# Optimization experiments

Measured on AMD Instinct MI355X. Metric: run time of the kernel, lower is better.

## Reference

```python
import jax, jax.numpy as jnp
import numpy as np

L1 = 512
LX = 32
COUNT = 8


def setup_inputs() -> dict:
    key = jax.random.key(0)
    ks = jax.random.split(key, 9)
    B = 65536
    x = jax.random.uniform(ks[0], (B, 2 * L1), dtype=jnp.float32)  # NNUE accumulator is in [0,1]
    ls_indices = jax.random.randint(ks[1], (B,), 0, COUNT, dtype=jnp.int64)
    # params (scaled ~1/sqrt(fan_in))
    w_fact = jax.random.normal(ks[2], (LX, 2 * L1), dtype=jnp.float32) * (1.0 / np.sqrt(2 * L1))
    w0 = jax.random.normal(ks[3], (LX * COUNT, 2 * L1), dtype=jnp.float32) * (1.0 / np.sqrt(2 * L1))
    b0 = jax.random.normal(ks[4], (LX * COUNT,), dtype=jnp.float32) * 0.05
    w1 = jax.random.normal(ks[5], (LX * COUNT, LX), dtype=jnp.float32) * (1.0 / np.sqrt(LX))
    b1 = jax.random.normal(ks[6], (LX * COUNT,), dtype=jnp.float32) * 0.05
    w2 = jax.random.normal(ks[7], (1 * COUNT, LX), dtype=jnp.float32) * (1.0 / np.sqrt(LX))
    b2 = jax.random.normal(ks[8], (1 * COUNT,), dtype=jnp.float32) * 0.05
    return {"x": x, "ls_indices": ls_indices, "w_fact": w_fact,
            "w0": w0, "b0": b0, "w1": w1, "b1": b1, "w2": w2, "b2": b2}


def _stack_linear_gather(h, w, b, idx, out_dim):
    # dense Linear for all COUNT buckets, then gather the selected bucket per row
    y = (h @ w.T + b).reshape(-1, COUNT, out_dim)          # [B, COUNT, out_dim]
    return y.reshape(-1, out_dim)[idx]                      # [B, out_dim]


def reference(x, ls_indices, w_fact, w0, b0, w1, b1, w2, b2):
    B = x.shape[0]
    idx = ls_indices.astype(jnp.int32) + jnp.arange(B, dtype=jnp.int32) * COUNT
    l1f = x @ w_fact.T                                      # [B, LX]
    h = _stack_linear_gather(x, w0, b0, idx, LX) + l1f      # layer 0 + factorized term
    h = jnp.clip(h, 0.0, 1.0)
    h = _stack_linear_gather(h, w1, b1, idx, LX)            # hidden layer 1
    h = jnp.clip(h, 0.0, 1.0)
    out = _stack_linear_gather(h, w2, b2, idx, 1)           # output layer (no clamp)
    return out
```

## Files before the change

### kernel.cpp

```cpp
#include <hip/hip_runtime.h>


#define B_ROWS 65536
#define LK     1024
#define TILE   32
#define MAIN_BLOCKS (B_ROWS / TILE + 8)
#define SROW   2056

#define SORTED_OFF 1024
#define WB_OFF     (1024 + 131072)

typedef short  short8  __attribute__((ext_vector_type(8)));
typedef float  f32x16  __attribute__((ext_vector_type(16)));

__device__ __forceinline__ unsigned pkbf(float a, float b) {
    unsigned ua = __float_as_uint(a), ub = __float_as_uint(b);
    ua = (ua + 0x7FFFu + ((ua >> 16) & 1u)) >> 16;
    ub = (ub + 0x7FFFu + ((ub >> 16) & 1u)) >> 16;
    return (ua & 0xFFFFu) | (ub << 16);
}

__device__ __forceinline__ bool detect_i64(const int* p) {
    int acc = 0;
#pragma unroll
    for (int i = 0; i < 64; ++i) acc |= p[2 * i + 1];
    return acc == 0;
}

__device__ __forceinline__ int load_bucket(const int* p, int r, bool i64) {
    return (i64 ? p[2 * r] : p[r]) & 7;
}

__global__ __launch_bounds__(1024) void k_prep(
    const int* __restrict__ idx, const float* __restrict__ w0,
    const float* __restrict__ wf, uint4* __restrict__ wB,
    unsigned short* __restrict__ sorted, int* __restrict__ hdr)
{
    int t = threadIdx.x;

    if (blockIdx.x > 0) {
        int f = (blockIdx.x - 1) * 1024 + t;
        int b   = f >> 12;
        int i12 = f & 4095;
        int kc  = i12 >> 8;
        int i8  = i12 & 255;
        int n   = i8 & 31;
        int khi = i8 >> 5;
        int k = kc * 64 + khi * 8;
        const float* p0 = w0 + (size_t)(b * 32 + n) * LK + k;
        const float* pf = wf + (size_t)n * LK + k;
        float v[8];
#pragma unroll
        for (int j = 0; j < 8; ++j) v[j] = p0[j] + pf[j];
        uint4 o;
        o.x = pkbf(v[0], v[1]); o.y = pkbf(v[2], v[3]);
        o.z = pkbf(v[4], v[5]); o.w = pkbf(v[6], v[7]);
        wB[f] = o;
        return;
    }

    __shared__ int wcnt[16][8];
    __shared__ int wbase[16][8];
    __shared__ int segb[8];

    bool i64 = detect_i64(idx);
    int wv = t >> 6, lane = t & 63;
    int rowbase = wv * 4096;

    unsigned nib[8] = {0, 0, 0, 0, 0, 0, 0, 0};
    int c[8] = {0, 0, 0, 0, 0, 0, 0, 0};
#pragma unroll 8
    for (int i = 0; i < 64; ++i) {
        int r = rowbase + i * 64 + lane;
        int b = load_bucket(idx, r, i64);
        nib[i >> 3] |= (unsigned)b << (4 * (i & 7));
#pragma unroll
        for (int bb = 0; bb < 8; ++bb) c[bb] += (b == bb) ? 1 : 0;
    }
#pragma unroll
    for (int bb = 0; bb < 8; ++bb) {
        int v = c[bb];
#pragma unroll
        for (int s = 1; s < 64; s <<= 1) v += __shfl_xor(v, s);
        if (lane == 0) wcnt[wv][bb] = v;
    }
    __syncthreads();

    if (t == 0) {
        int base = 0, tt = 0;
        for (int b = 0; b < 8; ++b) {
            int tot = 0;
            for (int w = 0; w < 16; ++w) tot += wcnt[w][b];
            hdr[b] = tot; hdr[16 + b] = base; hdr[24 + b] = tt;
            segb[b] = base;
            base += tot;
            tt += (tot + TILE - 1) / TILE;
        }
        hdr[24 + 8] = tt;
    }
    __syncthreads();

    if (t < 128) {
        int w2 = t >> 3, b = t & 7;
        int base = segb[b];
        for (int w = 0; w < w2; ++w) base += wcnt[w][b];
        wbase[w2][b] = base;
    }
    __syncthreads();

    int mycur = (lane < 8) ? wbase[wv][lane] : 0;
#pragma unroll
    for (int i = 0; i < 64; ++i) {
        int b = (nib[i >> 3] >> (4 * (i & 7))) & 7;
        unsigned long long mown = 0;
        int addc = 0;
#pragma unroll
        for (int bb = 0; bb < 8; ++bb) {
            unsigned long long m = __ballot(b == bb);
            if (b == bb) mown = m;
            if (lane == bb) addc = __popcll(m);
        }
        int base = __shfl(mycur, b);
        int rank = __popcll(mown & ((1ull << lane) - 1ull));
        sorted[base + rank] = (unsigned short)(rowbase + i * 64 + lane);
        mycur += addc;
    }
}

__global__ __launch_bounds__(256, 2) void k_main(
    const float* __restrict__ x, const unsigned short* __restrict__ sorted,
    const int* __restrict__ hdr, const uint4* __restrict__ wB,
    const float* __restrict__ b0, const float* __restrict__ w1,
    const float* __restrict__ b1, const float* __restrict__ w2,
    const float* __restrict__ b2, float* __restrict__ out)
{
    __shared__ __align__(16) unsigned char smem[TILE * SROW];
    float* rbuf = (float*)smem;
    float* hb   = (float*)(smem + 16384);

    int total = hdr[24 + 8];
    int g = blockIdx.x;
    if (g >= total) return;

    int bkt = 0;
    while (bkt < 7 && hdr[24 + bkt + 1] <= g) bkt++;
    int tile  = g - hdr[24 + bkt];
    int cnt   = hdr[bkt];
    int seg   = hdr[16 + bkt];
    int p0    = seg + tile * TILE;
    int nrows = min(TILE, cnt - tile * TILE);

    int t    = threadIdx.x;
    int lane = t & 63;
    int wv   = t >> 6;

#pragma unroll
    for (int j0 = 0; j0 < 32; j0 += 8) {
        float4 v[8];
#pragma unroll
        for (int jj = 0; jj < 8; ++jj) {
            int j = j0 + jj;
            int gr = (int)sorted[p0 + min(j, nrows - 1)];
            v[jj] = ((const float4*)(x + (size_t)gr * LK))[t];
        }
#pragma unroll
        for (int jj = 0; jj < 8; ++jj) {
            int j = j0 + jj;
            uint2 o;
            o.x = pkbf(v[jj].x, v[jj].y);
            o.y = pkbf(v[jj].z, v[jj].w);
            *(uint2*)(smem + j * SROW + t * 8) = o;
        }
    }
    __syncthreads();

    const uint4* wBg = wB + (size_t)bkt * 4096;
    const unsigned char* Abase = smem + (size_t)(lane & 31) * SROW + 16 * (lane >> 5);

    f32x16 acc;
#pragma unroll
    for (int i = 0; i < 16; ++i) acc[i] = 0.0f;

    union UA { uint2 h[2]; short8 s; };
    union UB { uint4 u;    short8 s; };
#pragma unroll
    for (int cc = 0; cc < 16; ++cc) {
        int c = wv * 16 + cc;
        UA ua;
        ua.h[0] = *(const uint2*)(Abase + 32 * c);
        ua.h[1] = *(const uint2*)(Abase + 32 * c + 8);
        UB ub;
        ub.u = wBg[c * 64 + lane];
        acc = __builtin_amdgcn_mfma_f32_32x32x16_bf16(ua.s, ub.s, acc, 0, 0, 0);
    }

    __syncthreads();
#pragma unroll
    for (int r = 0; r < 16; ++r)
        rbuf[wv * 1024 + r * 64 + lane] = acc[r];
    __syncthreads();

#pragma unroll
    for (int q = 0; q < 4; ++q) {
        int e = t + 256 * q;
        float s = rbuf[e] + rbuf[1024 + e] + rbuf[2048 + e] + rbuf[3072 + e];
        int rr = e >> 6, ll = e & 63;
        int m = (rr & 3) + 8 * (rr >> 2) + 4 * (ll >> 5);
        int n = ll & 31;
        float h = s + b0[bkt * 32 + n];
        h = fminf(fmaxf(h, 0.0f), 1.0f);
        hb[m * 36 + n] = h;
    }
    __syncthreads();

    if (t < 64) {
        int r = t >> 1, half = t & 1;
        const float4* hr = (const float4*)(hb + r * 36);
        float4 ha[8];
#pragma unroll
        for (int q = 0; q < 8; ++q) ha[q] = hr[q];
        const float* w1b = w1 + (size_t)bkt * 1024;
        const float* b1b = b1 + bkt * 32;
        const float* w2b = w2 + bkt * 32;
        float partial = 0.0f;
#pragma unroll
        for (int jj = 0; jj < 16; ++jj) {
            int j2 = half * 16 + jj;
            const float4* wr = (const float4*)&w1b[j2 * 32];
            float s = b1b[j2];
#pragma unroll
            for (int q = 0; q < 8; ++q) {
                float4 w4 = wr[q];
                s += ha[q].x * w4.x + ha[q].y * w4.y + ha[q].z * w4.z + ha[q].w * w4.w;
            }
            s = fminf(fmaxf(s, 0.0f), 1.0f);
            partial += s * w2b[j2];
        }
        partial += __shfl_xor(partial, 1);
        if (half == 0 && r < nrows) {
            int gr = (int)sorted[p0 + r];
            out[gr] = partial + b2[bkt];
        }
    }
}

extern "C" void kernel_launch(void* const* d_in, const int* in_sizes, int n_in,
                              void* d_out, int out_size, void* d_ws, size_t ws_size,
                              hipStream_t stream) {
    const float* x   = (const float*)d_in[0];
    const int*   lsi = (const int*)  d_in[1];
    const float* wf  = (const float*)d_in[2];
    const float* w0  = (const float*)d_in[3];
    const float* b0  = (const float*)d_in[4];
    const float* w1  = (const float*)d_in[5];
    const float* b1  = (const float*)d_in[6];
    const float* w2  = (const float*)d_in[7];
    const float* b2  = (const float*)d_in[8];
    float* out = (float*)d_out;

    char* ws = (char*)d_ws;
    int* hdr = (int*)ws;
    unsigned short* sorted = (unsigned short*)(ws + SORTED_OFF);
    uint4* wB = (uint4*)(ws + WB_OFF);

    k_prep<<<33, 1024, 0, stream>>>(lsi, w0, wf, wB, sorted, hdr);
    k_main<<<MAIN_BLOCKS, 256, 0, stream>>>(x, sorted, hdr, wB,
                                            b0, w1, b1, w2, b2, out);
}
```

Before: 439.1 us.

## Compute all buckets per tile in natural row order, dropping bucket sort

Removes the per-call bucket counting and sort of rows in the prep kernel. Each main-kernel block now processes 32 consecutive rows: every wave computes two buckets' layer-0 outputs over the full K, and each row keeps only its own bucket's result. This trades 8x more MFMA work and a full-K loop per wave for contiguous x loads, no gather, and no single-block sort step on the critical path. It also removes the cross-wave LDS reduction.

```diff
diff --git a/kernel.cpp b/kernel.cpp
--- a/kernel.cpp
+++ b/kernel.cpp
@@ -4,11 +4,9 @@
 #define B_ROWS 65536
 #define LK     1024
 #define TILE   32
-#define MAIN_BLOCKS (B_ROWS / TILE + 8)
+#define NBLK   (B_ROWS / TILE)
 #define SROW   2056
 
-#define SORTED_OFF 1024
-#define WB_OFF     (1024 + 131072)
 
 typedef short  short8  __attribute__((ext_vector_type(8)));
 typedef float  f32x16  __attribute__((ext_vector_type(16)));
@@ -32,189 +30,104 @@
 }
 
 __global__ __launch_bounds__(1024) void k_prep(
-    const int* __restrict__ idx, const float* __restrict__ w0,
-    const float* __restrict__ wf, uint4* __restrict__ wB,
-    unsigned short* __restrict__ sorted, int* __restrict__ hdr)
+    const float* __restrict__ w0, const float* __restrict__ wf,
+    uint4* __restrict__ wB)
 {
-    int t = threadIdx.x;
-
-    if (blockIdx.x > 0) {
-        int f = (blockIdx.x - 1) * 1024 + t;
-        int b   = f >> 12;
-        int i12 = f & 4095;
-        int kc  = i12 >> 8;
-        int i8  = i12 & 255;
-        int n   = i8 & 31;
-        int khi = i8 >> 5;
-        int k = kc * 64 + khi * 8;
-        const float* p0 = w0 + (size_t)(b * 32 + n) * LK + k;
-        const float* pf = wf + (size_t)n * LK + k;
-        float v[8];
+    int f = blockIdx.x * 1024 + threadIdx.x;
+    int b   = f >> 12;
+    int i12 = f & 4095;
+    int kc  = i12 >> 8;
+    int i8  = i12 & 255;
+    int n   = i8 & 31;
+    int khi = i8 >> 5;
+    int k = kc * 64 + khi * 8;
+    const float* p0 = w0 + (size_t)(b * 32 + n) * LK + k;
+    const float* pf = wf + (size_t)n * LK + k;
+    float v[8];
 #pragma unroll
-        for (int j = 0; j < 8; ++j) v[j] = p0[j] + pf[j];
-        uint4 o;
-        o.x = pkbf(v[0], v[1]); o.y = pkbf(v[2], v[3]);
-        o.z = pkbf(v[4], v[5]); o.w = pkbf(v[6], v[7]);
-        wB[f] = o;
-        return;
-    }
-
-    __shared__ int wcnt[16][8];
-    __shared__ int wbase[16][8];
-    __shared__ int segb[8];
-
-    bool i64 = detect_i64(idx);
-    int wv = t >> 6, lane = t & 63;
-    int rowbase = wv * 4096;
-
-    unsigned nib[8] = {0, 0, 0, 0, 0, 0, 0, 0};
-    int c[8] = {0, 0, 0, 0, 0, 0, 0, 0};
-#pragma unroll 8
-    for (int i = 0; i < 64; ++i) {
-        int r = rowbase + i * 64 + lane;
-        int b = load_bucket(idx, r, i64);
-        nib[i >> 3] |= (unsigned)b << (4 * (i & 7));
-#pragma unroll
-        for (int bb = 0; bb < 8; ++bb) c[bb] += (b == bb) ? 1 : 0;
-    }
-#pragma unroll
-    for (int bb = 0; bb < 8; ++bb) {
-        int v = c[bb];
-#pragma unroll
-        for (int s = 1; s < 64; s <<= 1) v += __shfl_xor(v, s);
-        if (lane == 0) wcnt[wv][bb] = v;
-    }
-    __syncthreads();
-
-    if (t == 0) {
-        int base = 0, tt = 0;
-        for (int b = 0; b < 8; ++b) {
-            int tot = 0;
-            for (int w = 0; w < 16; ++w) tot += wcnt[w][b];
-            hdr[b] = tot; hdr[16 + b] = base; hdr[24 + b] = tt;
-            segb[b] = base;
-            base += tot;
-            tt += (tot + TILE - 1) / TILE;
-        }
-        hdr[24 + 8] = tt;
-    }
-    __syncthreads();
-
-    if (t < 128) {
-        int w2 = t >> 3, b = t & 7;
-        int base = segb[b];
-        for (int w = 0; w < w2; ++w) base += wcnt[w][b];
-        wbase[w2][b] = base;
-    }
-    __syncthreads();
-
-    int mycur = (lane < 8) ? wbase[wv][lane] : 0;
-#pragma unroll
-    for (int i = 0; i < 64; ++i) {
-        int b = (nib[i >> 3] >> (4 * (i & 7))) & 7;
-        unsigned long long mown = 0;
-        int addc = 0;
-#pragma unroll
-        for (int bb = 0; bb < 8; ++bb) {
-            unsigned long long m = __ballot(b == bb);
-            if (b == bb) mown = m;
-            if (lane == bb) addc = __popcll(m);
-        }
-        int base = __shfl(mycur, b);
-        int rank = __popcll(mown & ((1ull << lane) - 1ull));
-        sorted[base + rank] = (unsigned short)(rowbase + i * 64 + lane);
-        mycur += addc;
-    }
+    for (int j = 0; j < 8; ++j) v[j] = p0[j] + pf[j];
+    uint4 o;
+    o.x = pkbf(v[0], v[1]); o.y = pkbf(v[2], v[3]);
+    o.z = pkbf(v[4], v[5]); o.w = pkbf(v[6], v[7]);
+    wB[f] = o;
 }
 
 __global__ __launch_bounds__(256, 2) void k_main(
-    const float* __restrict__ x, const unsigned short* __restrict__ sorted,
-    const int* __restrict__ hdr, const uint4* __restrict__ wB,
-    const float* __restrict__ b0, const float* __restrict__ w1,
-    const float* __restrict__ b1, const float* __restrict__ w2,
-    const float* __restrict__ b2, float* __restrict__ out)
+    const float* __restrict__ x, const int* __restrict__ idx,
+    const uint4* __restrict__ wB, const float* __restrict__ b0,
+    const float* __restrict__ w1, const float* __restrict__ b1,
+    const float* __restrict__ w2, const float* __restrict__ b2,
+    float* __restrict__ out)
 {
     __shared__ __align__(16) unsigned char smem[TILE * SROW];
-    float* rbuf = (float*)smem;
-    float* hb   = (float*)(smem + 16384);
+    __shared__ float hb[TILE * 36];
+    __shared__ int   bkt_s[TILE];
 
-    int total = hdr[24 + 8];
-    int g = blockIdx.x;
-    if (g >= total) return;
-
-    int bkt = 0;
-    while (bkt < 7 && hdr[24 + bkt + 1] <= g) bkt++;
-    int tile  = g - hdr[24 + bkt];
-    int cnt   = hdr[bkt];
-    int seg   = hdr[16 + bkt];
-    int p0    = seg + tile * TILE;
-    int nrows = min(TILE, cnt - tile * TILE);
-
+    int row0 = blockIdx.x * TILE;
     int t    = threadIdx.x;
     int lane = t & 63;
     int wv   = t >> 6;
+
+    if (t < TILE) {
+        bool i64 = detect_i64(idx);
+        bkt_s[t] = load_bucket(idx, row0 + t, i64);
+    }
 
 #pragma unroll
     for (int j0 = 0; j0 < 32; j0 += 8) {
         float4 v[8];
 #pragma unroll
-        for (int jj = 0; jj < 8; ++jj) {
-            int j = j0 + jj;
-            int gr = (int)sorted[p0 + min(j, nrows - 1)];
-            v[jj] = ((const float4*)(x + (size_t)gr * LK))[t];
-        }
+        for (int jj = 0; jj < 8; ++jj)
+            v[jj] = ((const float4*)(x + (size_t)(row0 + j0 + jj) * LK))[t];
 #pragma unroll
         for (int jj = 0; jj < 8; ++jj) {
-            int j = j0 + jj;
             uint2 o;
             o.x = pkbf(v[jj].x, v[jj].y);
             o.y = pkbf(v[jj].z, v[jj].w);
-            *(uint2*)(smem + j * SROW + t * 8) = o;
+            *(uint2*)(smem + (j0 + jj) * SROW + t * 8) = o;
         }
     }
     __syncthreads();
 
-    const uint4* wBg = wB + (size_t)bkt * 4096;
+    const uint4* wB0 = wB + (size_t)(2 * wv) * 4096;
+    const uint4* wB1 = wB + (size_t)(2 * wv + 1) * 4096;
     const unsigned char* Abase = smem + (size_t)(lane & 31) * SROW + 16 * (lane >> 5);
 
-    f32x16 acc;
+    f32x16 acc0, acc1;
 #pragma unroll
-    for (int i = 0; i < 16; ++i) acc[i] = 0.0f;
+    for (int i = 0; i < 16; ++i) { acc0[i] = 0.0f; acc1[i] = 0.0f; }
 
     union UA { uint2 h[2]; short8 s; };
     union UB { uint4 u;    short8 s; };
-#pragma unroll
-    for (int cc = 0; cc < 16; ++cc) {
-        int c = wv * 16 + cc;
+#pragma unroll 4
+    for (int c = 0; c < 64; ++c) {
         UA ua;
         ua.h[0] = *(const uint2*)(Abase + 32 * c);
         ua.h[1] = *(const uint2*)(Abase + 32 * c + 8);
-        UB ub;
-        ub.u = wBg[c * 64 + lane];
-        acc = __builtin_amdgcn_mfma_f32_32x32x16_bf16(ua.s, ub.s, acc, 0, 0, 0);
+        UB ub0, ub1;
+        ub0.u = wB0[c * 64 + lane];
+        ub1.u = wB1[c * 64 + lane];
+        acc0 = __builtin_amdgcn_mfma_f32_32x32x16_bf16(ua.s, ub0.s, acc0, 0, 0, 0);
+        acc1 = __builtin_amdgcn_mfma_f32_32x32x16_bf16(ua.s, ub1.s, acc1, 0, 0, 0);
     }
 
-    __syncthreads();
+    int bb0 = 2 * wv, bb1 = 2 * wv + 1;
 #pragma unroll
-    for (int r = 0; r < 16; ++r)
-        rbuf[wv * 1024 + r * 64 + lane] = acc[r];
-    __syncthreads();
-
-#pragma unroll
-    for (int q = 0; q < 4; ++q) {
-        int e = t + 256 * q;
-        float s = rbuf[e] + rbuf[1024 + e] + rbuf[2048 + e] + rbuf[3072 + e];
-        int rr = e >> 6, ll = e & 63;
-        int m = (rr & 3) + 8 * (rr >> 2) + 4 * (ll >> 5);
-        int n = ll & 31;
-        float h = s + b0[bkt * 32 + n];
-        h = fminf(fmaxf(h, 0.0f), 1.0f);
-        hb[m * 36 + n] = h;
+    for (int i = 0; i < 16; ++i) {
+        int m = (i & 3) + 8 * (i >> 2) + 4 * (lane >> 5);
+        int n = lane & 31;
+        int mb = bkt_s[m];
+        if (mb == bb0 || mb == bb1) {
+            float s = (mb == bb0) ? acc0[i] : acc1[i];
+            float h = s + b0[mb * 32 + n];
+            hb[m * 36 + n] = fminf(fmaxf(h, 0.0f), 1.0f);
+        }
     }
     __syncthreads();
 
     if (t < 64) {
         int r = t >> 1, half = t & 1;
+        int bkt = bkt_s[r];
         const float4* hr = (const float4*)(hb + r * 36);
         float4 ha[8];
 #pragma unroll
@@ -237,10 +150,7 @@
             partial += s * w2b[j2];
         }
         partial += __shfl_xor(partial, 1);
-        if (half == 0 && r < nrows) {
-            int gr = (int)sorted[p0 + r];
-            out[gr] = partial + b2[bkt];
-        }
+        if (half == 0) out[row0 + r] = partial + b2[bkt];
     }
 }
 
@@ -258,12 +168,8 @@
     const float* b2  = (const float*)d_in[8];
     float* out = (float*)d_out;
 
-    char* ws = (char*)d_ws;
-    int* hdr = (int*)ws;
-    unsigned short* sorted = (unsigned short*)(ws + SORTED_OFF);
-    uint4* wB = (uint4*)(ws + WB_OFF);
+    uint4* wB = (uint4*)d_ws;
 
-    k_prep<<<33, 1024, 0, stream>>>(lsi, w0, wf, wB, sorted, hdr);
-    k_main<<<MAIN_BLOCKS, 256, 0, stream>>>(x, sorted, hdr, wB,
-                                            b0, w1, b1, w2, b2, out);
+    k_prep<<<32, 1024, 0, stream>>>(w0, wf, wB);
+    k_main<<<NBLK, 256, 0, stream>>>(x, lsi, wB, b0, w1, b1, w2, b2, out);
 }
```

New measurement: 451.8 us. 2.9% more time.
